# Performance work log

Measured on AMD Instinct MI355X. Metric: run time of the kernel, lower is better.

The kernel has to match this reference:

```python
import jax, jax.numpy as jnp
import numpy as np

N_NODES = 100000
N_EDGES = 800000
N_REL = 16
D = 64
EPS = 1e-12
NEG_SLOPE = 0.01  # nn.LeakyReLU default


def _l2norm(x):
    # matches torch F.normalize(p=2, dim=-1)
    n = jnp.sqrt(jnp.sum(x * x, axis=-1, keepdims=True))
    return x / jnp.maximum(n, EPS)


def setup_inputs() -> dict:
    key = jax.random.key(0)
    ks = jax.random.split(key, 12)
    inp = {
        "src": jax.random.randint(ks[0], (N_EDGES,), 0, N_NODES, dtype=jnp.int32),
        "dst": jax.random.randint(ks[1], (N_EDGES,), 0, N_NODES, dtype=jnp.int32),
        "etype": jax.random.randint(ks[2], (N_EDGES,), 0, N_REL, dtype=jnp.int32),
        "ent_embed": jax.random.normal(ks[3], (N_NODES, D), jnp.float32) * 0.1,
        "ent_transfer": jax.random.normal(ks[4], (N_NODES, D), jnp.float32) * 0.1,
        "rel_embed": jax.random.normal(ks[5], (N_REL, D), jnp.float32) * 0.1,
        "rel_transfer": jax.random.normal(ks[6], (N_REL, D), jnp.float32) * 0.1,
        "W1_0": jax.random.normal(ks[7], (64, 32), jnp.float32) * (1.0 / np.sqrt(64)),
        "b1_0": jnp.zeros((32,), jnp.float32),
        "W2_0": jax.random.normal(ks[8], (64, 32), jnp.float32) * (1.0 / np.sqrt(64)),
        "b2_0": jnp.zeros((32,), jnp.float32),
        "W1_1": jax.random.normal(ks[9], (32, 16), jnp.float32) * (1.0 / np.sqrt(32)),
        "b1_1": jnp.zeros((16,), jnp.float32),
        "W2_1": jax.random.normal(ks[10], (32, 16), jnp.float32) * (1.0 / np.sqrt(32)),
        "b2_1": jnp.zeros((16,), jnp.float32),
    }
    return inp


def _compute_att(src, dst, etype, ent_embed, ent_transfer, rel_embed, rel_transfer):
    # per-edge gathers: h = dst node, t = src node (KGAT att_score convention)
    h_e = ent_embed[dst]          # [E, D]
    t_e = ent_embed[src]          # [E, D]
    h_p = ent_transfer[dst]
    t_p = ent_transfer[src]
    r_p = rel_transfer[etype]     # [E, D]
    r_e = rel_embed[etype]        # [E, D]
    # TransD projection + L2 normalize
    Mrt = _l2norm(t_e + jnp.sum(t_e * t_p, -1, keepdims=True) * r_p)
    Mrh = _l2norm(h_e + jnp.sum(h_e * h_p, -1, keepdims=True) * r_p)
    att = jnp.sum(Mrt * jnp.tanh(Mrh + r_e), axis=-1)  # [E]
    # edge softmax grouped by destination node
    m = jax.ops.segment_max(att, dst, num_segments=N_NODES)
    m = jnp.where(jnp.isfinite(m), m, 0.0)
    ex = jnp.exp(att - m[dst])
    s = jax.ops.segment_sum(ex, dst, num_segments=N_NODES)
    return ex / jnp.maximum(s[dst], EPS)  # [E]


def _bi_layer(node, N_h, W1, b1, W2, b2):
    out1 = jax.nn.leaky_relu((node + N_h) @ W1 + b1, NEG_SLOPE)
    out2 = jax.nn.leaky_relu((node * N_h) @ W2 + b2, NEG_SLOPE)
    return out1 + out2


def reference(src, dst, etype, ent_embed, ent_transfer, rel_embed, rel_transfer,
              W1_0, b1_0, W2_0, b2_0, W1_1, b1_1, W2_1, b2_1):
    att = _compute_att(src, dst, etype, ent_embed, ent_transfer, rel_embed, rel_transfer)
    node = ent_embed
    all_embed = [node]
    for (W1, b1, W2, b2) in [(W1_0, b1_0, W2_0, b2_0), (W1_1, b1_1, W2_1, b2_1)]:
        # u_mul_e + sum: N_h[v] = sum_{e: dst(e)=v} att_e * node[src(e)]
        msg = att[:, None] * node[src]                      # [E, d]
        N_h = jax.ops.segment_sum(msg, dst, num_segments=N_NODES)
        node = _bi_layer(node, N_h, W1, b1, W2, b2)         # dropout p=0 (eval)
        all_embed.append(_l2norm(node))
    return jnp.concatenate(all_embed, axis=1)  # [N, 64+32+16]
```

## Files before the change

kernel.cpp:

```cpp
#include <hip/hip_runtime.h>
#include <math.h>

#define EPSF 1e-12f
#define LOG2E 1.44269504f

__device__ __forceinline__ float red16(float v) {
    v += __shfl_xor(v, 1, 16);
    v += __shfl_xor(v, 2, 16);
    v += __shfl_xor(v, 4, 16);
    v += __shfl_xor(v, 8, 16);
    return v;
}

__device__ __forceinline__ float red8(float v) {
    v += __shfl_xor(v, 1, 8);
    v += __shfl_xor(v, 2, 8);
    v += __shfl_xor(v, 4, 8);
    return v;
}

__device__ __forceinline__ float fast_tanh(float x) {
    float E = __builtin_amdgcn_exp2f(x * (2.0f * LOG2E));
    return 1.0f - 2.0f * __builtin_amdgcn_rcpf(E + 1.0f);
}

__device__ __forceinline__ float inv_norm(float x) {
    return __builtin_amdgcn_rsqf(fmaxf(x, 1e-24f));
}

__device__ __forceinline__ float leaky(float x) {
    return x > 0.0f ? x : 0.01f * x;
}

__global__ __launch_bounds__(256) void precomp_dot(
    const float* __restrict__ ent, const float* __restrict__ entT,
    float* __restrict__ dot, int N) {
    int gid = blockIdx.x * 256 + threadIdx.x;
    int v = gid >> 4, lane = gid & 15;
    if (v >= N) return;
    const float4 a = *(const float4*)(ent  + (size_t)v * 64 + lane * 4);
    const float4 b = *(const float4*)(entT + (size_t)v * 64 + lane * 4);
    float d = red16(a.x*b.x + a.y*b.y + a.z*b.z + a.w*b.w);
    if (lane == 0) dot[v] = d;
}


__global__ __launch_bounds__(256) void count_deg(
    const int* __restrict__ dst, int* __restrict__ deg, int E) {
    int e = blockIdx.x * 256 + threadIdx.x;
    if (e < E) atomicAdd(&deg[dst[e]], 1);
}

__global__ __launch_bounds__(256) void scan_reduce(
    const int* __restrict__ deg, int* __restrict__ part, int N) {
    __shared__ int sh[256];
    int t = threadIdx.x, i = blockIdx.x * 256 + t;
    sh[t] = (i < N) ? deg[i] : 0;
    __syncthreads();
    for (int off = 128; off > 0; off >>= 1) {
        if (t < off) sh[t] += sh[t + off];
        __syncthreads();
    }
    if (t == 0) part[blockIdx.x] = sh[0];
}

__global__ __launch_bounds__(1024) void scan_part(int* __restrict__ part, int nb) {
    __shared__ int sh[1024];
    int t = threadIdx.x;
    int x = (t < nb) ? part[t] : 0;
    sh[t] = x;
    __syncthreads();
    for (int off = 1; off < 1024; off <<= 1) {
        int y = (t >= off) ? sh[t - off] : 0;
        __syncthreads();
        sh[t] += y;
        __syncthreads();
    }
    if (t < nb) part[t] = sh[t] - x;
}

__global__ __launch_bounds__(256) void scan_write(
    int* __restrict__ rowptr, const int* __restrict__ part, int N) {
    __shared__ int sh[256];
    int t = threadIdx.x, i = blockIdx.x * 256 + t;
    int x = (i < N) ? rowptr[i] : 0;
    sh[t] = x;
    __syncthreads();
    for (int off = 1; off < 256; off <<= 1) {
        int y = (t >= off) ? sh[t - off] : 0;
        __syncthreads();
        sh[t] += y;
        __syncthreads();
    }
    if (i < N) rowptr[i] = part[blockIdx.x] + sh[t] - x;
}

__global__ __launch_bounds__(256) void scatter_edges(
    const int* __restrict__ src, const int* __restrict__ dst,
    const int* __restrict__ ety, int* __restrict__ rowptr,
    int* __restrict__ spk, int E) {
    int e = blockIdx.x * 256 + threadIdx.x;
    if (e < E) {
        int slot = atomicAdd(&rowptr[dst[e]], 1);
        spk[slot] = src[e] | (ety[e] << 20);
    }
}

__global__ __launch_bounds__(256) void fused_l0(
    const int* __restrict__ rowptr, const int* __restrict__ spk,
    const float* __restrict__ ent, const float* __restrict__ dot,
    const float* __restrict__ relE, const float* __restrict__ relT,
    const float* __restrict__ W1, const float* __restrict__ b1,
    const float* __restrict__ W2, const float* __restrict__ b2,
    float* __restrict__ exatt, float* __restrict__ sinv,
    float* __restrict__ node1raw, float* __restrict__ out, int N) {
    __shared__ float al[16][68];
    __shared__ float bl[16][68];
    __shared__ float rT[16][68];
    __shared__ float rE[16][68];
    int t = threadIdx.x;

    {
        int r = t >> 4, c = (t & 15) * 4;
        *(float4*)&rT[r][c] = *(const float4*)(relT + r * 64 + c);
        *(float4*)&rE[r][c] = *(const float4*)(relE + r * 64 + c);
    }
    __syncthreads();

    int nv = t >> 4, lane = t & 15;
    int v = blockIdx.x * 16 + nv;
    if (v >= N) return;

    int s = v ? rowptr[v - 1] : 0;
    int epos = rowptr[v];
    const float4 he = *(const float4*)(ent + (size_t)v * 64 + lane * 4);
    float dh = dot[v];

    float4 macc = {0.f, 0.f, 0.f, 0.f};
    float sumex = 0.0f;

    for (int base = s; base < epos; base += 16) {
        int rem = epos - base;
        int cnt = rem < 16 ? rem : 16;
        int mypk = spk[base + (lane < rem ? lane : rem - 1)];

        int pk0 = __shfl(mypk, 0, 16);
        int pk1 = __shfl(mypk, cnt > 1 ? 1 : 0, 16);
        float4 te0 = *(const float4*)(ent + (size_t)(pk0 & 0xFFFFF) * 64 + lane * 4);
        float  sd0 = dot[pk0 & 0xFFFFF];
        float4 te1 = *(const float4*)(ent + (size_t)(pk1 & 0xFFFFF) * 64 + lane * 4);
        float  sd1 = dot[pk1 & 0xFFFFF];

        for (int k = 0; k < cnt; k += 2) {
            float4 ta = te0, tb = te1;
            float  sa = sd0, sb = sd1;
            int rva = (pk0 >> 20) & 15;
            int rvb = (pk1 >> 20) & 15;
            bool hasb = (k + 1) < cnt;

            if (k + 2 < cnt) {
                pk0 = __shfl(mypk, k + 2, 16);
                pk1 = __shfl(mypk, (k + 3 < cnt) ? (k + 3) : (k + 2), 16);
                te0 = *(const float4*)(ent + (size_t)(pk0 & 0xFFFFF) * 64 + lane * 4);
                sd0 = dot[pk0 & 0xFFFFF];
                te1 = *(const float4*)(ent + (size_t)(pk1 & 0xFFFFF) * 64 + lane * 4);
                sd1 = dot[pk1 & 0xFFFFF];
            }

            const float4 rpa = *(const float4*)&rT[rva][lane * 4];
            const float4 rea = *(const float4*)&rE[rva][lane * 4];
            const float4 rpb = *(const float4*)&rT[rvb][lane * 4];
            const float4 reb = *(const float4*)&rE[rvb][lane * 4];

            float4 mta, mha, mtb, mhb;
            mta.x = ta.x + sa * rpa.x; mta.y = ta.y + sa * rpa.y;
            mta.z = ta.z + sa * rpa.z; mta.w = ta.w + sa * rpa.w;
            mha.x = he.x + dh * rpa.x; mha.y = he.y + dh * rpa.y;
            mha.z = he.z + dh * rpa.z; mha.w = he.w + dh * rpa.w;
            mtb.x = tb.x + sb * rpb.x; mtb.y = tb.y + sb * rpb.y;
            mtb.z = tb.z + sb * rpb.z; mtb.w = tb.w + sb * rpb.w;
            mhb.x = he.x + dh * rpb.x; mhb.y = he.y + dh * rpb.y;
            mhb.z = he.z + dh * rpb.z; mhb.w = he.w + dh * rpb.w;

            float ssta = red16(mta.x*mta.x + mta.y*mta.y + mta.z*mta.z + mta.w*mta.w);
            float ssha = red16(mha.x*mha.x + mha.y*mha.y + mha.z*mha.z + mha.w*mha.w);
            float sstb = red16(mtb.x*mtb.x + mtb.y*mtb.y + mtb.z*mtb.z + mtb.w*mtb.w);
            float sshb = red16(mhb.x*mhb.x + mhb.y*mhb.y + mhb.z*mhb.z + mhb.w*mhb.w);
            float ita = inv_norm(ssta), iha = inv_norm(ssha);
            float itb = inv_norm(sstb), ihb = inv_norm(sshb);

            float txa = fast_tanh(mha.x * iha + rea.x);
            float tya = fast_tanh(mha.y * iha + rea.y);
            float tza = fast_tanh(mha.z * iha + rea.z);
            float twa = fast_tanh(mha.w * iha + rea.w);
            float txb = fast_tanh(mhb.x * ihb + reb.x);
            float tyb = fast_tanh(mhb.y * ihb + reb.y);
            float tzb = fast_tanh(mhb.z * ihb + reb.z);
            float twb = fast_tanh(mhb.w * ihb + reb.w);

            float atta = ita * red16(mta.x*txa + mta.y*tya + mta.z*tza + mta.w*twa);
            float attb = itb * red16(mtb.x*txb + mtb.y*tyb + mtb.z*tzb + mtb.w*twb);

            float exa  = __builtin_amdgcn_exp2f(atta * LOG2E);
            float exbR = __builtin_amdgcn_exp2f(attb * LOG2E);
            float exb  = hasb ? exbR : 0.0f;

            if (lane == 0) {
                exatt[base + k] = exa;
                if (hasb) exatt[base + k + 1] = exbR;
            }
            sumex += exa + exb;
            macc.x += exa * ta.x + exb * tb.x;
            macc.y += exa * ta.y + exb * tb.y;
            macc.z += exa * ta.z + exb * tb.z;
            macc.w += exa * ta.w + exb * tb.w;
        }
    }

    float inv = 1.0f / fmaxf(sumex, EPSF);
    if (lane == 0) sinv[v] = inv;
    macc.x *= inv; macc.y *= inv; macc.z *= inv; macc.w *= inv;

    *(float4*)(out + (size_t)v * 112 + lane * 4) = he;

    float4 av, bv;
    av.x = he.x + macc.x; av.y = he.y + macc.y;
    av.z = he.z + macc.z; av.w = he.w + macc.w;
    bv.x = he.x * macc.x; bv.y = he.y * macc.y;
    bv.z = he.z * macc.z; bv.w = he.w * macc.w;
    *(float4*)&al[nv][lane * 4] = av;
    *(float4*)&bl[nv][lane * 4] = bv;

    #pragma unroll
    for (int jo = 0; jo < 2; ++jo) {
        int j = lane + jo * 16;
        float acc1 = b1[j], acc2 = b2[j];
        #pragma unroll
        for (int d = 0; d < 64; d += 4) {
            float4 a4 = *(const float4*)&al[nv][d];
            float4 b4 = *(const float4*)&bl[nv][d];
            acc1 += a4.x * W1[(d+0)*32 + j] + a4.y * W1[(d+1)*32 + j]
                  + a4.z * W1[(d+2)*32 + j] + a4.w * W1[(d+3)*32 + j];
            acc2 += b4.x * W2[(d+0)*32 + j] + b4.y * W2[(d+1)*32 + j]
                  + b4.z * W2[(d+2)*32 + j] + b4.w * W2[(d+3)*32 + j];
        }
        node1raw[(size_t)v * 32 + j] = leaky(acc1) + leaky(acc2);
    }
}

__global__ __launch_bounds__(256) void fused_l1(
    const int* __restrict__ rowptr, const int* __restrict__ spk,
    const float* __restrict__ exatt, const float* __restrict__ sinv,
    const float* __restrict__ node1raw,
    const float* __restrict__ W1, const float* __restrict__ b1,
    const float* __restrict__ W2, const float* __restrict__ b2,
    float* __restrict__ out, int N) {
    __shared__ float A[32][36];
    __shared__ float B[32][36];
    int t = threadIdx.x;
    int nv = t >> 3, lane = t & 7;
    int v = blockIdx.x * 32 + nv;
    if (v >= N) return;

    int s = v ? rowptr[v - 1] : 0;
    int epos = rowptr[v];
    float4 n = *(const float4*)(node1raw + (size_t)v * 32 + lane * 4);
    float4 acc = {0.f, 0.f, 0.f, 0.f};

    for (int base = s; base < epos; base += 8) {
        int rem = epos - base;
        int cnt = rem < 8 ? rem : 8;
        int idx = base + (lane < rem ? lane : rem - 1);
        int   mypk = spk[idx];
        float myex = exatt[idx];

        int pk0 = __shfl(mypk, 0, 8);
        int pk1 = __shfl(mypk, cnt > 1 ? 1 : 0, 8);
        float4 x0 = *(const float4*)(node1raw + (size_t)(pk0 & 0xFFFFF) * 32 + lane * 4);
        float4 x1 = *(const float4*)(node1raw + (size_t)(pk1 & 0xFFFFF) * 32 + lane * 4);

        for (int k = 0; k < cnt; k += 2) {
            float4 xa = x0, xb = x1;
            float aa = __shfl(myex, k, 8);
            float ab = __shfl(myex, (k + 1 < cnt) ? (k + 1) : k, 8);
            if (!((k + 1) < cnt)) ab = 0.0f;

            if (k + 2 < cnt) {
                pk0 = __shfl(mypk, k + 2, 8);
                pk1 = __shfl(mypk, (k + 3 < cnt) ? (k + 3) : (k + 2), 8);
                x0 = *(const float4*)(node1raw + (size_t)(pk0 & 0xFFFFF) * 32 + lane * 4);
                x1 = *(const float4*)(node1raw + (size_t)(pk1 & 0xFFFFF) * 32 + lane * 4);
            }
            acc.x += aa * xa.x + ab * xb.x;
            acc.y += aa * xa.y + ab * xb.y;
            acc.z += aa * xa.z + ab * xb.z;
            acc.w += aa * xa.w + ab * xb.w;
        }
    }
    float inv = sinv[v];
    acc.x *= inv; acc.y *= inv; acc.z *= inv; acc.w *= inv;

    float ss = red8(n.x*n.x + n.y*n.y + n.z*n.z + n.w*n.w);
    float inv1 = inv_norm(ss);
    float4 nn = {n.x*inv1, n.y*inv1, n.z*inv1, n.w*inv1};
    *(float4*)(out + (size_t)v * 112 + 64 + lane * 4) = nn;

    float4 av = {n.x + acc.x, n.y + acc.y, n.z + acc.z, n.w + acc.w};
    float4 bv = {n.x * acc.x, n.y * acc.y, n.z * acc.z, n.w * acc.w};
    *(float4*)&A[nv][lane * 4] = av;
    *(float4*)&B[nv][lane * 4] = bv;

    int j0 = lane * 2;
    float a10 = b1[j0], a11 = b1[j0 + 1];
    float a20 = b2[j0], a21 = b2[j0 + 1];
    #pragma unroll
    for (int d = 0; d < 32; d += 4) {
        float4 a4 = *(const float4*)&A[nv][d];
        float4 b4 = *(const float4*)&B[nv][d];
        float2 w0 = *(const float2*)(W1 + (d+0)*16 + j0);
        float2 w1 = *(const float2*)(W1 + (d+1)*16 + j0);
        float2 w2 = *(const float2*)(W1 + (d+2)*16 + j0);
        float2 w3 = *(const float2*)(W1 + (d+3)*16 + j0);
        a10 += a4.x*w0.x + a4.y*w1.x + a4.z*w2.x + a4.w*w3.x;
        a11 += a4.x*w0.y + a4.y*w1.y + a4.z*w2.y + a4.w*w3.y;
        float2 u0 = *(const float2*)(W2 + (d+0)*16 + j0);
        float2 u1 = *(const float2*)(W2 + (d+1)*16 + j0);
        float2 u2 = *(const float2*)(W2 + (d+2)*16 + j0);
        float2 u3 = *(const float2*)(W2 + (d+3)*16 + j0);
        a20 += b4.x*u0.x + b4.y*u1.x + b4.z*u2.x + b4.w*u3.x;
        a21 += b4.x*u0.y + b4.y*u1.y + b4.z*u2.y + b4.w*u3.y;
    }
    float t0 = leaky(a10) + leaky(a20);
    float t1 = leaky(a11) + leaky(a21);
    float s2 = red8(t0*t0 + t1*t1);
    float inv2 = inv_norm(s2);
    float2 o = {t0 * inv2, t1 * inv2};
    *(float2*)(out + (size_t)v * 112 + 96 + j0) = o;
}

extern "C" void kernel_launch(void* const* d_in, const int* in_sizes, int n_in,
                              void* d_out, int out_size, void* d_ws, size_t ws_size,
                              hipStream_t stream) {
    const int*   src  = (const int*)d_in[0];
    const int*   dst  = (const int*)d_in[1];
    const int*   ety  = (const int*)d_in[2];
    const float* ent  = (const float*)d_in[3];
    const float* entT = (const float*)d_in[4];
    const float* relE = (const float*)d_in[5];
    const float* relT = (const float*)d_in[6];
    const float* W1_0 = (const float*)d_in[7];
    const float* b1_0 = (const float*)d_in[8];
    const float* W2_0 = (const float*)d_in[9];
    const float* b2_0 = (const float*)d_in[10];
    const float* W1_1 = (const float*)d_in[11];
    const float* b1_1 = (const float*)d_in[12];
    const float* W2_1 = (const float*)d_in[13];
    const float* b2_1 = (const float*)d_in[14];
    float* out = (float*)d_out;

    const int E = in_sizes[0];
    const int N = in_sizes[3] / 64;
    const int nb = (N + 255) / 256;

    auto al256 = [](size_t x) { return (x + 255) & ~(size_t)255; };
    char* ws = (char*)d_ws;
    size_t offExatt = 0;
    size_t offS     = al256(offExatt + (size_t)E * 4);
    size_t offDot   = al256(offS + (size_t)N * 4);
    size_t offRow   = al256(offDot + (size_t)N * 4);
    size_t offSpk   = al256(offRow + (size_t)N * 4);
    size_t offPart  = al256(offSpk + (size_t)E * 4);
    size_t offN1    = al256(offPart + (size_t)nb * 4);
    float* exatt    = (float*)(ws + offExatt);
    float* sinv     = (float*)(ws + offS);
    float* dot      = (float*)(ws + offDot);
    int*   rowptr   = (int*)(ws + offRow);
    int*   spk      = (int*)(ws + offSpk);
    int*   part     = (int*)(ws + offPart);
    float* node1raw = (float*)(ws + offN1);

    hipMemsetAsync(rowptr, 0, (size_t)N * 4, stream);
    precomp_dot<<<(N * 16 + 255) / 256, 256, 0, stream>>>(ent, entT, dot, N);
    int blkE = (E + 255) / 256;
    count_deg<<<blkE, 256, 0, stream>>>(dst, rowptr, E);
    scan_reduce<<<nb, 256, 0, stream>>>(rowptr, part, N);
    scan_part<<<1, 1024, 0, stream>>>(part, nb);
    scan_write<<<nb, 256, 0, stream>>>(rowptr, part, N);
    scatter_edges<<<blkE, 256, 0, stream>>>(src, dst, ety, rowptr, spk, E);

    fused_l0<<<(N + 15) / 16, 256, 0, stream>>>(
        rowptr, spk, ent, dot, relE, relT,
        W1_0, b1_0, W2_0, b2_0, exatt, sinv, node1raw, out, N);

    fused_l1<<<(N + 31) / 32, 256, 0, stream>>>(
        rowptr, spk, exatt, sinv, node1raw,
        W1_1, b1_1, W2_1, b2_1, out, N);
}
```

Baseline: 246.9 us.

## Split each node's edge list across two lane groups and merge prep kernels

Both aggregation kernels now assign two lane groups per destination node. Each group walks half of the incoming edges, and the partial sums are combined with a cross-half shuffle. The goal is more memory-level parallelism on the latency-bound gathers and shorter serial edge loops per node. As a consequence, fewer nodes fit in each block, and the matvec epilogue runs one output column per thread. The dot-product precompute and degree counting are also fused into a single launch to save one kernel launch. A risk is that a barrier-free LDS handoff between the two halves now spans wavefront-half boundaries within the same wave.

```diff
diff --git a/kernel.cpp b/kernel.cpp
--- a/kernel.cpp
+++ b/kernel.cpp
@@ -32,24 +32,23 @@
     return x > 0.0f ? x : 0.01f * x;
 }
 
-__global__ __launch_bounds__(256) void precomp_dot(
+__global__ __launch_bounds__(256) void prep(
     const float* __restrict__ ent, const float* __restrict__ entT,
-    float* __restrict__ dot, int N) {
+    float* __restrict__ dot, const int* __restrict__ dst,
+    int* __restrict__ deg, int N16, int E) {
     int gid = blockIdx.x * 256 + threadIdx.x;
-    int v = gid >> 4, lane = gid & 15;
-    if (v >= N) return;
-    const float4 a = *(const float4*)(ent  + (size_t)v * 64 + lane * 4);
-    const float4 b = *(const float4*)(entT + (size_t)v * 64 + lane * 4);
-    float d = red16(a.x*b.x + a.y*b.y + a.z*b.z + a.w*b.w);
-    if (lane == 0) dot[v] = d;
-}
-
-
-__global__ __launch_bounds__(256) void count_deg(
-    const int* __restrict__ dst, int* __restrict__ deg, int E) {
-    int e = blockIdx.x * 256 + threadIdx.x;
-    if (e < E) atomicAdd(&deg[dst[e]], 1);
-}
+    if (gid < N16) {
+        int v = gid >> 4, lane = gid & 15;
+        const float4 a = *(const float4*)(ent  + (size_t)v * 64 + lane * 4);
+        const float4 b = *(const float4*)(entT + (size_t)v * 64 + lane * 4);
+        float d = red16(a.x*b.x + a.y*b.y + a.z*b.z + a.w*b.w);
+        if (lane == 0) dot[v] = d;
+    } else {
+        int e = gid - N16;
+        if (e < E) atomicAdd(&deg[dst[e]], 1);
+    }
+}
+
 
 __global__ __launch_bounds__(256) void scan_reduce(
     const int* __restrict__ deg, int* __restrict__ part, int N) {
@@ -114,8 +113,8 @@
     const float* __restrict__ W2, const float* __restrict__ b2,
     float* __restrict__ exatt, float* __restrict__ sinv,
     float* __restrict__ node1raw, float* __restrict__ out, int N) {
-    __shared__ float al[16][68];
-    __shared__ float bl[16][68];
+    __shared__ float al[8][68];
+    __shared__ float bl[8][68];
     __shared__ float rT[16][68];
     __shared__ float rE[16][68];
     int t = threadIdx.x;
@@ -127,20 +126,25 @@
     }
     __syncthreads();
 
-    int nv = t >> 4, lane = t & 15;
-    int v = blockIdx.x * 16 + nv;
+    int nv = t >> 5, half = (t >> 4) & 1, lane = t & 15;
+    int v = blockIdx.x * 8 + nv;
     if (v >= N) return;
 
     int s = v ? rowptr[v - 1] : 0;
     int epos = rowptr[v];
+    int deg = epos - s;
+    int mid = s + ((deg + 1) >> 1);
+    int hs   = half ? mid  : s;
+    int hend = half ? epos : mid;
+
     const float4 he = *(const float4*)(ent + (size_t)v * 64 + lane * 4);
     float dh = dot[v];
 
     float4 macc = {0.f, 0.f, 0.f, 0.f};
     float sumex = 0.0f;
 
-    for (int base = s; base < epos; base += 16) {
-        int rem = epos - base;
+    for (int base = hs; base < hend; base += 16) {
+        int rem = hend - base;
         int cnt = rem < 16 ? rem : 16;
         int mypk = spk[base + (lane < rem ? lane : rem - 1)];
 
@@ -217,35 +221,39 @@
         }
     }
 
+    sumex  += __shfl_xor(sumex,  16, 32);
+    macc.x += __shfl_xor(macc.x, 16, 32);
+    macc.y += __shfl_xor(macc.y, 16, 32);
+    macc.z += __shfl_xor(macc.z, 16, 32);
+    macc.w += __shfl_xor(macc.w, 16, 32);
+
     float inv = 1.0f / fmaxf(sumex, EPSF);
-    if (lane == 0) sinv[v] = inv;
+    if ((t & 31) == 0) sinv[v] = inv;
     macc.x *= inv; macc.y *= inv; macc.z *= inv; macc.w *= inv;
 
-    *(float4*)(out + (size_t)v * 112 + lane * 4) = he;
-
-    float4 av, bv;
-    av.x = he.x + macc.x; av.y = he.y + macc.y;
-    av.z = he.z + macc.z; av.w = he.w + macc.w;
-    bv.x = he.x * macc.x; bv.y = he.y * macc.y;
-    bv.z = he.z * macc.z; bv.w = he.w * macc.w;
-    *(float4*)&al[nv][lane * 4] = av;
-    *(float4*)&bl[nv][lane * 4] = bv;
-
+    if (!half) {
+        *(float4*)(out + (size_t)v * 112 + lane * 4) = he;
+        float4 av, bv;
+        av.x = he.x + macc.x; av.y = he.y + macc.y;
+        av.z = he.z + macc.z; av.w = he.w + macc.w;
+        bv.x = he.x * macc.x; bv.y = he.y * macc.y;
+        bv.z = he.z * macc.z; bv.w = he.w * macc.w;
+        *(float4*)&al[nv][lane * 4] = av;
+        *(float4*)&bl[nv][lane * 4] = bv;
+    }
+
+    int j = t & 31;
+    float acc1 = b1[j], acc2 = b2[j];
     #pragma unroll
-    for (int jo = 0; jo < 2; ++jo) {
-        int j = lane + jo * 16;
-        float acc1 = b1[j], acc2 = b2[j];
-        #pragma unroll
-        for (int d = 0; d < 64; d += 4) {
-            float4 a4 = *(const float4*)&al[nv][d];
-            float4 b4 = *(const float4*)&bl[nv][d];
-            acc1 += a4.x * W1[(d+0)*32 + j] + a4.y * W1[(d+1)*32 + j]
-                  + a4.z * W1[(d+2)*32 + j] + a4.w * W1[(d+3)*32 + j];
-            acc2 += b4.x * W2[(d+0)*32 + j] + b4.y * W2[(d+1)*32 + j]
-                  + b4.z * W2[(d+2)*32 + j] + b4.w * W2[(d+3)*32 + j];
-        }
-        node1raw[(size_t)v * 32 + j] = leaky(acc1) + leaky(acc2);
-    }
+    for (int d = 0; d < 64; d += 4) {
+        float4 a4 = *(const float4*)&al[nv][d];
+        float4 b4 = *(const float4*)&bl[nv][d];
+        acc1 += a4.x * W1[(d+0)*32 + j] + a4.y * W1[(d+1)*32 + j]
+              + a4.z * W1[(d+2)*32 + j] + a4.w * W1[(d+3)*32 + j];
+        acc2 += b4.x * W2[(d+0)*32 + j] + b4.y * W2[(d+1)*32 + j]
+              + b4.z * W2[(d+2)*32 + j] + b4.w * W2[(d+3)*32 + j];
+    }
+    node1raw[(size_t)v * 32 + j] = leaky(acc1) + leaky(acc2);
 }
 
 __global__ __launch_bounds__(256) void fused_l1(
@@ -255,20 +263,25 @@
     const float* __restrict__ W1, const float* __restrict__ b1,
     const float* __restrict__ W2, const float* __restrict__ b2,
     float* __restrict__ out, int N) {
-    __shared__ float A[32][36];
-    __shared__ float B[32][36];
+    __shared__ float A[16][36];
+    __shared__ float B[16][36];
     int t = threadIdx.x;
-    int nv = t >> 3, lane = t & 7;
-    int v = blockIdx.x * 32 + nv;
+    int nv = t >> 4, half = (t >> 3) & 1, lane = t & 7;
+    int v = blockIdx.x * 16 + nv;
     if (v >= N) return;
 
     int s = v ? rowptr[v - 1] : 0;
     int epos = rowptr[v];
+    int deg = epos - s;
+    int mid = s + ((deg + 1) >> 1);
+    int hs   = half ? mid  : s;
+    int hend = half ? epos : mid;
+
     float4 n = *(const float4*)(node1raw + (size_t)v * 32 + lane * 4);
     float4 acc = {0.f, 0.f, 0.f, 0.f};
 
-    for (int base = s; base < epos; base += 8) {
-        int rem = epos - base;
+    for (int base = hs; base < hend; base += 8) {
+        int rem = hend - base;
         int cnt = rem < 8 ? rem : 8;
         int idx = base + (lane < rem ? lane : rem - 1);
         int   mypk = spk[idx];
@@ -297,45 +310,41 @@
             acc.w += aa * xa.w + ab * xb.w;
         }
     }
+    acc.x += __shfl_xor(acc.x, 8, 16);
+    acc.y += __shfl_xor(acc.y, 8, 16);
+    acc.z += __shfl_xor(acc.z, 8, 16);
+    acc.w += __shfl_xor(acc.w, 8, 16);
+
     float inv = sinv[v];
     acc.x *= inv; acc.y *= inv; acc.z *= inv; acc.w *= inv;
 
     float ss = red8(n.x*n.x + n.y*n.y + n.z*n.z + n.w*n.w);
     float inv1 = inv_norm(ss);
-    float4 nn = {n.x*inv1, n.y*inv1, n.z*inv1, n.w*inv1};
-    *(float4*)(out + (size_t)v * 112 + 64 + lane * 4) = nn;
-
-    float4 av = {n.x + acc.x, n.y + acc.y, n.z + acc.z, n.w + acc.w};
-    float4 bv = {n.x * acc.x, n.y * acc.y, n.z * acc.z, n.w * acc.w};
-    *(float4*)&A[nv][lane * 4] = av;
-    *(float4*)&B[nv][lane * 4] = bv;
-
-    int j0 = lane * 2;
-    float a10 = b1[j0], a11 = b1[j0 + 1];
-    float a20 = b2[j0], a21 = b2[j0 + 1];
+
+    if (!half) {
+        float4 nn = {n.x*inv1, n.y*inv1, n.z*inv1, n.w*inv1};
+        *(float4*)(out + (size_t)v * 112 + 64 + lane * 4) = nn;
+        float4 av = {n.x + acc.x, n.y + acc.y, n.z + acc.z, n.w + acc.w};
+        float4 bv = {n.x * acc.x, n.y * acc.y, n.z * acc.z, n.w * acc.w};
+        *(float4*)&A[nv][lane * 4] = av;
+        *(float4*)&B[nv][lane * 4] = bv;
+    }
+
+    int j = t & 15;
+    float a1 = b1[j], a2 = b2[j];
     #pragma unroll
     for (int d = 0; d < 32; d += 4) {
         float4 a4 = *(const float4*)&A[nv][d];
         float4 b4 = *(const float4*)&B[nv][d];
-        float2 w0 = *(const float2*)(W1 + (d+0)*16 + j0);
-        float2 w1 = *(const float2*)(W1 + (d+1)*16 + j0);
-        float2 w2 = *(const float2*)(W1 + (d+2)*16 + j0);
-        float2 w3 = *(const float2*)(W1 + (d+3)*16 + j0);
-        a10 += a4.x*w0.x + a4.y*w1.x + a4.z*w2.x + a4.w*w3.x;
-        a11 += a4.x*w0.y + a4.y*w1.y + a4.z*w2.y + a4.w*w3.y;
-        float2 u0 = *(const float2*)(W2 + (d+0)*16 + j0);
-        float2 u1 = *(const float2*)(W2 + (d+1)*16 + j0);
-        float2 u2 = *(const float2*)(W2 + (d+2)*16 + j0);
-        float2 u3 = *(const float2*)(W2 + (d+3)*16 + j0);
-        a20 += b4.x*u0.x + b4.y*u1.x + b4.z*u2.x + b4.w*u3.x;
-        a21 += b4.x*u0.y + b4.y*u1.y + b4.z*u2.y + b4.w*u3.y;
-    }
-    float t0 = leaky(a10) + leaky(a20);
-    float t1 = leaky(a11) + leaky(a21);
-    float s2 = red8(t0*t0 + t1*t1);
+        a1 += a4.x * W1[(d+0)*16 + j] + a4.y * W1[(d+1)*16 + j]
+            + a4.z * W1[(d+2)*16 + j] + a4.w * W1[(d+3)*16 + j];
+        a2 += b4.x * W2[(d+0)*16 + j] + b4.y * W2[(d+1)*16 + j]
+            + b4.z * W2[(d+2)*16 + j] + b4.w * W2[(d+3)*16 + j];
+    }
+    float tot = leaky(a1) + leaky(a2);
+    float s2 = red16(tot * tot);
     float inv2 = inv_norm(s2);
-    float2 o = {t0 * inv2, t1 * inv2};
-    *(float2*)(out + (size_t)v * 112 + 96 + j0) = o;
+    out[(size_t)v * 112 + 96 + j] = tot * inv2;
 }
 
 extern "C" void kernel_launch(void* const* d_in, const int* in_sizes, int n_in,
@@ -380,19 +389,20 @@
     float* node1raw = (float*)(ws + offN1);
 
     hipMemsetAsync(rowptr, 0, (size_t)N * 4, stream);
-    precomp_dot<<<(N * 16 + 255) / 256, 256, 0, stream>>>(ent, entT, dot, N);
-    int blkE = (E + 255) / 256;
-    count_deg<<<blkE, 256, 0, stream>>>(dst, rowptr, E);
+    int N16 = N * 16;
+    prep<<<(N16 + E + 255) / 256, 256, 0, stream>>>(ent, entT, dot, dst,
+                                                    rowptr, N16, E);
     scan_reduce<<<nb, 256, 0, stream>>>(rowptr, part, N);
     scan_part<<<1, 1024, 0, stream>>>(part, nb);
     scan_write<<<nb, 256, 0, stream>>>(rowptr, part, N);
+    int blkE = (E + 255) / 256;
     scatter_edges<<<blkE, 256, 0, stream>>>(src, dst, ety, rowptr, spk, E);
 
-    fused_l0<<<(N + 15) / 16, 256, 0, stream>>>(
+    fused_l0<<<(N + 7) / 8, 256, 0, stream>>>(
         rowptr, spk, ent, dot, relE, relT,
         W1_0, b1_0, W2_0, b2_0, exatt, sinv, node1raw, out, N);
 
-    fused_l1<<<(N + 31) / 32, 256, 0, stream>>>(
+    fused_l1<<<(N + 15) / 16, 256, 0, stream>>>(
         rowptr, spk, exatt, sinv, node1raw,
         W1_1, b1_1, W2_1, b2_1, out, N);
 }
```

Result: faster. 231.0 us (-6.5%).
